# Kernel tuning notes

Measured on AMD Instinct MI355X. Metric: run time of the kernel, lower is better.

The kernel has to match this reference:

```python
import jax, jax.numpy as jnp
import numpy as np

D_MODEL = 768
NUM_HEADS = 12
HEAD_DIM = D_MODEL // NUM_HEADS  # 64, also rotary dim
INTERMEDIATE = 1152
WINDOW = 128          # config.local_attention (layer_id=1 -> local layer)
ROPE_BASE = 10000.0   # local_rope_theta
EPS = 1e-5


def layer_norm_nocenter(x, gamma):
    # keras LayerNormalization(center=False): mean-subtract, no beta
    mu = jnp.mean(x, axis=-1, keepdims=True)
    var = jnp.var(x, axis=-1, keepdims=True)
    return (x - mu) * jax.lax.rsqrt(var + EPS) * gamma


def rotate_half(x):
    x1, x2 = jnp.split(x, 2, axis=-1)
    return jnp.concatenate([-x2, x1], axis=-1)


def setup_inputs() -> dict:
    key = jax.random.key(0)
    ks = jax.random.split(key, 7)
    B, S = 4, 2048
    hidden_states = jax.random.normal(ks[0], (B, S, D_MODEL), dtype=jnp.float32)
    attention_mask = jnp.zeros((B, 1, S, S), dtype=jnp.float32)  # no padding
    s = 0.02
    attn_norm_gamma = jnp.ones((D_MODEL,), dtype=jnp.float32)
    wqkv = jax.random.normal(ks[1], (D_MODEL, 3 * D_MODEL), dtype=jnp.float32) * s
    wo_attn = jax.random.normal(ks[2], (D_MODEL, D_MODEL), dtype=jnp.float32) * s
    mlp_norm_gamma = jnp.ones((D_MODEL,), dtype=jnp.float32)
    wi = jax.random.normal(ks[3], (D_MODEL, 2 * INTERMEDIATE), dtype=jnp.float32) * s
    wo_mlp = jax.random.normal(ks[4], (INTERMEDIATE, D_MODEL), dtype=jnp.float32) * s
    return {
        'hidden_states': hidden_states,
        'attention_mask': attention_mask,
        'attn_norm_gamma': attn_norm_gamma,
        'wqkv': wqkv,
        'wo_attn': wo_attn,
        'mlp_norm_gamma': mlp_norm_gamma,
        'wi': wi,
        'wo_mlp': wo_mlp,
    }


def reference(hidden_states, attention_mask, attn_norm_gamma, wqkv, wo_attn,
              mlp_norm_gamma, wi, wo_mlp):
    B, S, Dm = hidden_states.shape
    H, Dh = NUM_HEADS, HEAD_DIM

    # RoPE cache (NTKScaling with scaling_factor=1 -> plain RoPE)
    idx = jnp.arange(0, Dh, 2, dtype=jnp.float32)
    inv_freq = 1.0 / (ROPE_BASE ** (idx / Dh))          # [Dh/2]
    t = jnp.arange(S, dtype=jnp.float32)
    freqs = t[:, None] * inv_freq[None, :]              # [S, Dh/2]
    emb = jnp.concatenate([freqs, freqs], axis=-1)      # [S, Dh]
    cos = jnp.cos(emb)[None, None]                      # [1,1,S,Dh]
    sin = jnp.sin(emb)[None, None]

    # combined sliding-window + padding mask
    pos = jnp.arange(S)
    dist = jnp.abs(pos[:, None] - pos[None, :])
    neg = jnp.finfo(jnp.float32).min
    local = jnp.where(dist <= WINDOW // 2, 0.0, neg).astype(jnp.float32)
    mask = attention_mask + local[None, None]           # [B,1,S,S]

    # attention (layer_id != 0 -> pre-norm)
    x = layer_norm_nocenter(hidden_states, attn_norm_gamma)
    qkv = (x @ wqkv).reshape(B, S, 3, H, Dh).transpose(2, 0, 3, 1, 4)
    q, k, v = qkv[0], qkv[1], qkv[2]                    # [B,H,S,Dh]
    q = q * cos + rotate_half(q) * sin
    k = k * cos + rotate_half(k) * sin

    scale = 1.0 / jnp.sqrt(jnp.asarray(Dh, q.dtype))
    scores = jnp.einsum('bhqd,bhkd->bhqk', q, k) * scale + mask
    attn = jax.nn.softmax(scores, axis=-1)
    ctx = jnp.einsum('bhqk,bhkd->bhqd', attn, v)
    attn_out = ctx.transpose(0, 2, 1, 3).reshape(B, S, Dm) @ wo_attn

    h = hidden_states + attn_out

    # GLU MLP: Wi -> split -> gelu(x)*gate -> Wo, residual
    n = layer_norm_nocenter(h, mlp_norm_gamma)
    x_in, gate = jnp.split(n @ wi, 2, axis=-1)
    mlp = jax.nn.gelu(x_in, approximate=False) * gate
    return h + mlp @ wo_mlp
```

## Files before the change

### kernel.cpp

```cpp
#include <hip/hip_runtime.h>
#include <cstdint>
#include <cstddef>

typedef __bf16 bf16;
typedef float f32x4 __attribute__((ext_vector_type(4)));
typedef __bf16 bf16x8 __attribute__((ext_vector_type(8)));
typedef __bf16 bf16x4 __attribute__((ext_vector_type(4)));

#define MFMA16(a, b, c) __builtin_amdgcn_mfma_f32_16x16x32_bf16((a), (b), (c), 0, 0, 0)

__device__ __forceinline__ void gload_lds16(const void* g, void* l) {
  __builtin_amdgcn_global_load_lds((__attribute__((address_space(1))) void*)g,
                                   (__attribute__((address_space(3))) void*)l,
                                   16, 0, 0);
}

__global__ __launch_bounds__(256) void wconv_all(const float* __restrict__ wqkv,
                                                 const float* __restrict__ woa,
                                                 const float* __restrict__ wi,
                                                 const float* __restrict__ wom,
                                                 bf16* __restrict__ wqkvT,
                                                 bf16* __restrict__ woaT,
                                                 bf16* __restrict__ wiIT,
                                                 bf16* __restrict__ womT) {
  int id = blockIdx.x;
  const float* W;
  bf16* Wt;
  int K, N, bx, by;
  bool inter = false;
  if (id < 1728) { W = wqkv; Wt = wqkvT; K = 768; N = 2304; bx = id % 72; by = id / 72; }
  else if (id < 2304) { id -= 1728; W = woa; Wt = woaT; K = 768; N = 768; bx = id % 24; by = id / 24; }
  else if (id < 4032) { id -= 2304; W = wi; Wt = wiIT; K = 768; N = 2304; inter = true; bx = id % 72; by = id / 72; }
  else { id -= 4032; W = wom; Wt = womT; K = 1152; N = 768; bx = id % 24; by = id / 24; }

  __shared__ float tile[32][33];
  const int n0 = bx * 32, k0 = by * 32;
  const int t = threadIdx.x;
  const int c = t & 31, r = t >> 5;
#pragma unroll
  for (int i = 0; i < 4; ++i)
    tile[r + i * 8][c] = W[(size_t)(k0 + r + i * 8) * N + n0 + c];
  __syncthreads();
#pragma unroll
  for (int i = 0; i < 4; ++i) {
    int n = n0 + r + i * 8;
    int nw = inter ? ((n < 1152) ? 2 * n : 2 * (n - 1152) + 1) : n;
    Wt[(size_t)nw * K + k0 + c] = (bf16)tile[c][r + i * 8];
  }
}

__global__ __launch_bounds__(256) void ln_kernel(const float* __restrict__ X,
                                                 const float* __restrict__ gamma,
                                                 bf16* __restrict__ out) {
  const int row = blockIdx.x, t = threadIdx.x;
  const float* xr = X + (size_t)row * 768;
  float v0 = xr[t], v1 = xr[t + 256], v2 = xr[t + 512];
  float s = v0 + v1 + v2;
  float s2 = v0 * v0 + v1 * v1 + v2 * v2;
#pragma unroll
  for (int m = 1; m <= 32; m <<= 1) {
    s += __shfl_xor(s, m, 64);
    s2 += __shfl_xor(s2, m, 64);
  }
  __shared__ float red[8];
  const int w = t >> 6, lane = t & 63;
  if (lane == 0) { red[w] = s; red[4 + w] = s2; }
  __syncthreads();
  s = red[0] + red[1] + red[2] + red[3];
  s2 = red[4] + red[5] + red[6] + red[7];
  const float mu = s * (1.f / 768.f);
  const float var = s2 * (1.f / 768.f) - mu * mu;
  const float rs = rsqrtf(var + 1e-5f);
  out[(size_t)row * 768 + t] = (bf16)((v0 - mu) * rs * gamma[t]);
  out[(size_t)row * 768 + t + 256] = (bf16)((v1 - mu) * rs * gamma[t + 256]);
  out[(size_t)row * 768 + t + 512] = (bf16)((v2 - mu) * rs * gamma[t + 512]);
}

template <int BM, bool RES, typename TOUT>
__global__ __launch_bounds__(256) void gemm_bt(const bf16* __restrict__ A,
                                               const bf16* __restrict__ Bt,
                                               const float* __restrict__ Res,
                                               TOUT* __restrict__ C, int M, int N, int K) {
  constexpr int MT = BM / 32;
  __shared__ __align__(16) bf16 As[BM * 64];
  __shared__ __align__(16) bf16 Bs[128 * 64];
  const int t = threadIdx.x;
  const int lane = t & 63;
  const int w = t >> 6;
  const int wm = w >> 1, wn = w & 1;
  const int row0 = blockIdx.y * BM, col0 = blockIdx.x * 128;
  const int rm = lane & 15, qd = lane >> 4;
  f32x4 acc[MT][4] = {};
  for (int k0 = 0; k0 < K; k0 += 64) {
#pragma unroll
    for (int i = 0; i < BM / 32; ++i) {
      int c = i * 256 + t;
      int r = c >> 3, j = (c & 7) ^ (r & 7);
      gload_lds16(A + (size_t)(row0 + r) * K + (k0 + j * 8), &As[c * 8]);
    }
#pragma unroll
    for (int i = 0; i < 4; ++i) {
      int c = i * 256 + t;
      int r = c >> 3, j = (c & 7) ^ (r & 7);
      gload_lds16(Bt + (size_t)(col0 + r) * K + (k0 + j * 8), &Bs[c * 8]);
    }
    __syncthreads();
#pragma unroll
    for (int kb = 0; kb < 2; ++kb) {
      bf16x8 af[MT], bfr[4];
#pragma unroll
      for (int mt = 0; mt < MT; ++mt) {
        int r = wm * (MT * 16) + mt * 16 + rm;
        af[mt] = *(const bf16x8*)&As[r * 64 + (((kb * 4 + qd) ^ (r & 7)) * 8)];
      }
#pragma unroll
      for (int nt = 0; nt < 4; ++nt) {
        int r = wn * 64 + nt * 16 + rm;
        bfr[nt] = *(const bf16x8*)&Bs[r * 64 + (((kb * 4 + qd) ^ (r & 7)) * 8)];
      }
#pragma unroll
      for (int mt = 0; mt < MT; ++mt)
#pragma unroll
        for (int nt = 0; nt < 4; ++nt)
          acc[mt][nt] = MFMA16(af[mt], bfr[nt], acc[mt][nt]);
    }
    __syncthreads();
  }
#pragma unroll
  for (int mt = 0; mt < MT; ++mt)
#pragma unroll
    for (int nt = 0; nt < 4; ++nt) {
      const int gc = col0 + wn * 64 + nt * 16 + rm;
#pragma unroll
      for (int r = 0; r < 4; ++r) {
        const int gr = row0 + wm * (MT * 16) + mt * 16 + qd * 4 + r;
        float v = acc[mt][nt][r];
        const size_t idx = (size_t)gr * N + gc;
        if (RES) v += Res[idx];
        C[idx] = (TOUT)v;
      }
    }
}

__global__ __launch_bounds__(256) void gemm_wi(const bf16* __restrict__ A,
                                               const bf16* __restrict__ Bt,
                                               bf16* __restrict__ outp) {
  __shared__ __align__(16) bf16 As[128 * 64];
  __shared__ __align__(16) bf16 Bs[128 * 64];
  const int t = threadIdx.x;
  const int lane = t & 63;
  const int w = t >> 6;
  const int wm = w >> 1, wn = w & 1;
  const int row0 = blockIdx.y * 128, col0 = blockIdx.x * 128;
  const int rm = lane & 15, qd = lane >> 4;
  f32x4 acc[4][4] = {};
  for (int k0 = 0; k0 < 768; k0 += 64) {
#pragma unroll
    for (int i = 0; i < 4; ++i) {
      int c = i * 256 + t;
      int r = c >> 3, j = (c & 7) ^ (r & 7);
      gload_lds16(A + (size_t)(row0 + r) * 768 + (k0 + j * 8), &As[c * 8]);
      gload_lds16(Bt + (size_t)(col0 + r) * 768 + (k0 + j * 8), &Bs[c * 8]);
    }
    __syncthreads();
#pragma unroll
    for (int kb = 0; kb < 2; ++kb) {
      bf16x8 af[4], bfr[4];
#pragma unroll
      for (int mt = 0; mt < 4; ++mt) {
        int r = wm * 64 + mt * 16 + rm;
        af[mt] = *(const bf16x8*)&As[r * 64 + (((kb * 4 + qd) ^ (r & 7)) * 8)];
      }
#pragma unroll
      for (int nt = 0; nt < 4; ++nt) {
        int r = wn * 64 + nt * 16 + rm;
        bfr[nt] = *(const bf16x8*)&Bs[r * 64 + (((kb * 4 + qd) ^ (r & 7)) * 8)];
      }
#pragma unroll
      for (int mt = 0; mt < 4; ++mt)
#pragma unroll
        for (int nt = 0; nt < 4; ++nt)
          acc[mt][nt] = MFMA16(af[mt], bfr[nt], acc[mt][nt]);
    }
    __syncthreads();
  }
#pragma unroll
  for (int mt = 0; mt < 4; ++mt)
#pragma unroll
    for (int nt = 0; nt < 4; ++nt) {
      const int ci = col0 + wn * 64 + nt * 16 + rm;
#pragma unroll
      for (int r = 0; r < 4; ++r) {
        const int gr = row0 + wm * 64 + mt * 16 + qd * 4 + r;
        float v = acc[mt][nt][r];
        float other = __shfl_xor(v, 1, 64);
        if ((rm & 1) == 0) {
          float x = v, g = other;
          float ge = 0.5f * x * (1.0f + erff(x * 0.70710678118654752f));
          outp[(size_t)gr * 1152 + (ci >> 1)] = (bf16)(ge * g);
        }
      }
    }
}

__global__ __launch_bounds__(256) void gemm_qkv(const bf16* __restrict__ A,
                                                const bf16* __restrict__ Bt,
                                                bf16* __restrict__ Qb,
                                                bf16* __restrict__ Kb,
                                                bf16* __restrict__ Vt) {
  __shared__ __align__(16) bf16 SM[17408];
  bf16* As = SM;
  bf16* Bs = SM + 8192;

  const int t = threadIdx.x;
  const int lane = t & 63;
  const int w = t >> 6;
  const int wm = w >> 1, wn = w & 1;
  const int row0 = blockIdx.y * 128, col0 = blockIdx.x * 128;
  const int rm = lane & 15, qd = lane >> 4;
  f32x4 acc[4][4] = {};
  for (int k0 = 0; k0 < 768; k0 += 64) {
#pragma unroll
    for (int i = 0; i < 4; ++i) {
      int c = i * 256 + t;
      int r = c >> 3, j = (c & 7) ^ (r & 7);
      gload_lds16(A + (size_t)(row0 + r) * 768 + (k0 + j * 8), &As[c * 8]);
      gload_lds16(Bt + (size_t)(col0 + r) * 768 + (k0 + j * 8), &Bs[c * 8]);
    }
    __syncthreads();
#pragma unroll
    for (int kb = 0; kb < 2; ++kb) {
      bf16x8 af[4], bfr[4];
#pragma unroll
      for (int mt = 0; mt < 4; ++mt) {
        int r = wm * 64 + mt * 16 + rm;
        af[mt] = *(const bf16x8*)&As[r * 64 + (((kb * 4 + qd) ^ (r & 7)) * 8)];
      }
#pragma unroll
      for (int nt = 0; nt < 4; ++nt) {
        int r = wn * 64 + nt * 16 + rm;
        bfr[nt] = *(const bf16x8*)&Bs[r * 64 + (((kb * 4 + qd) ^ (r & 7)) * 8)];
      }
#pragma unroll
      for (int mt = 0; mt < 4; ++mt)
#pragma unroll
        for (int nt = 0; nt < 4; ++nt)
          acc[mt][nt] = MFMA16(af[mt], bfr[nt], acc[mt][nt]);
    }
    __syncthreads();
  }

  const int head_id = blockIdx.x * 2 + wn;
  const int typ = blockIdx.x / 6;
  const int b = row0 >> 11;
  const int sblk = row0 & 2047;
  const int sw = sblk + wm * 64;

  if (typ < 2) {
    const int h = head_id - typ * 12;
    const size_t bhbase = (size_t)(b * 12 + h) * 2048;
    bf16* dst = typ ? Kb : Qb;
    float invf[2];
#pragma unroll
    for (int nt = 0; nt < 2; ++nt)
      invf[nt] = exp2f((float)(nt * 16 + rm) * -0.41524101186092029f);
#pragma unroll
    for (int mt = 0; mt < 4; ++mt)
#pragma unroll
      for (int r = 0; r < 4; ++r) {
        int s = sw + mt * 16 + qd * 4 + r;
#pragma unroll
        for (int nt = 0; nt < 2; ++nt) {
          float ang = (float)s * invf[nt];
          float rev = ang * 0.15915494309189535f;
          rev -= floorf(rev);
          float sn = __builtin_amdgcn_sinf(rev);
          float cs = __builtin_amdgcn_cosf(rev);
          float x1 = acc[mt][nt][r], x2 = acc[mt][nt + 2][r];
          int d = nt * 16 + rm;
          dst[(bhbase + s) * 64 + d] = (bf16)(x1 * cs - x2 * sn);
          dst[(bhbase + s) * 64 + d + 32] = (bf16)(x2 * cs + x1 * sn);
        }
      }
  } else {
#pragma unroll
    for (int mt = 0; mt < 4; ++mt)
#pragma unroll
      for (int nt = 0; nt < 4; ++nt) {
        int hd = wn * 64 + nt * 16 + rm;
        int sl = wm * 64 + mt * 16 + qd * 4;
        bf16x4 v4;
#pragma unroll
        for (int r = 0; r < 4; ++r) v4[r] = (bf16)acc[mt][nt][r];
        *(bf16x4*)&SM[hd * 136 + sl] = v4;
      }
    __syncthreads();
    const int h0 = blockIdx.x * 2 - 24;
#pragma unroll
    for (int it = 0; it < 8; ++it) {
      int cc = it * 256 + t;
      int hd = cc >> 4, s8 = (cc & 15) * 8;
      bf16x8 vv = *(const bf16x8*)&SM[hd * 136 + s8];
      size_t grow = (size_t)(b * 12 + h0 + (hd >> 6)) * 64 + (hd & 63);
      *(bf16x8*)&Vt[grow * 2048 + sblk + s8] = vv;
    }
  }
}

__global__ __launch_bounds__(256) void attn_kernel(const bf16* __restrict__ Qb,
                                                   const bf16* __restrict__ Kb,
                                                   const bf16* __restrict__ Vt,
                                                   const float* __restrict__ am,
                                                   bf16* __restrict__ ctx) {
  __shared__ __align__(16) bf16 KP[64 * 200];
  __shared__ __align__(16) bf16 Vts[64 * 192];
  bf16* Ks = KP;
  bf16* Ps = KP;

  const int t = threadIdx.x;
  const int lane = t & 63, w = t >> 6;
  const int rm = lane & 15, qd = lane >> 4;
  const int s0 = blockIdx.x * 64;
  const int bh = blockIdx.y;
  const int b = bh / 12, h = bh - b * 12;
  const size_t baseQ = (size_t)bh * 2048;

#pragma unroll
  for (int i = 0; i < 6; ++i) {
    int c = i * 256 + t;
    int r = c >> 3, j = (c & 7) ^ (r & 7);
    int key = min(max(s0 - 64 + r, 0), 2047);
    gload_lds16(Kb + (baseQ + key) * 64 + j * 8, &Ks[c * 8]);
  }
#pragma unroll
  for (int i = 0; i < 6; ++i) {
    int c = i * 256 + t;
    int r = c / 24, jl = c - r * 24;
    int j = (jl & 24) | ((jl & 7) ^ (r & 7));
    int k0 = min(max(s0 - 64 + j * 8, 0), 2040);
    gload_lds16(Vt + ((size_t)bh * 64 + r) * 2048 + k0, &Vts[c * 8]);
  }

  bf16x8 aq[2];
#pragma unroll
  for (int kb = 0; kb < 2; ++kb)
    aq[kb] = *(const bf16x8*)&Qb[(baseQ + s0 + w * 16 + rm) * 64 + kb * 32 + qd * 8];

  float msk[12][4];
#pragma unroll
  for (int nt = 0; nt < 12; ++nt) {
    int key = s0 - 64 + nt * 16 + rm;
#pragma unroll
    for (int r = 0; r < 4; ++r) {
      int qpos = s0 + w * 16 + qd * 4 + r;
      bool valid = (key >= 0) && (key < 2048) && (key - qpos <= 64) && (qpos - key <= 64);
      msk[nt][r] = valid ? am[((size_t)b * 2048 + qpos) * 2048 + key] : -3e38f;
    }
  }
  __syncthreads();

  f32x4 sc[12];
#pragma unroll
  for (int nt = 0; nt < 12; ++nt) {
    f32x4 a = {0.f, 0.f, 0.f, 0.f};
#pragma unroll
    for (int kb = 0; kb < 2; ++kb) {
      int r = nt * 16 + rm;
      bf16x8 bk = *(const bf16x8*)&Ks[r * 64 + (((kb * 4 + qd) ^ (rm & 7)) * 8)];
      a = MFMA16(aq[kb], bk, a);
    }
    sc[nt] = a;
  }

  float mx[4] = {-3e38f, -3e38f, -3e38f, -3e38f};
#pragma unroll
  for (int nt = 0; nt < 12; ++nt)
#pragma unroll
    for (int r = 0; r < 4; ++r) {
      float v = (msk[nt][r] <= -2.9e38f) ? -3e38f : sc[nt][r] * 0.125f + msk[nt][r];
      sc[nt][r] = v;
      mx[r] = fmaxf(mx[r], v);
    }
#pragma unroll
  for (int r = 0; r < 4; ++r)
#pragma unroll
    for (int m = 1; m <= 8; m <<= 1) mx[r] = fmaxf(mx[r], __shfl_xor(mx[r], m, 64));
  float sum[4] = {0.f, 0.f, 0.f, 0.f};
#pragma unroll
  for (int nt = 0; nt < 12; ++nt)
#pragma unroll
    for (int r = 0; r < 4; ++r) {
      float p = (sc[nt][r] > -1e37f) ? __expf(sc[nt][r] - mx[r]) : 0.f;
      sc[nt][r] = p;
      sum[r] += p;
    }
#pragma unroll
  for (int r = 0; r < 4; ++r)
#pragma unroll
    for (int m = 1; m <= 8; m <<= 1) sum[r] += __shfl_xor(sum[r], m, 64);
  float inv[4];
#pragma unroll
  for (int r = 0; r < 4; ++r) inv[r] = 1.f / sum[r];

  __syncthreads();

#pragma unroll
  for (int nt = 0; nt < 12; ++nt)
#pragma unroll
    for (int r = 0; r < 4; ++r)
      Ps[(w * 16 + qd * 4 + r) * 200 + nt * 16 + rm] = (bf16)(sc[nt][r] * inv[r]);

  f32x4 o[4] = {};
#pragma unroll
  for (int ks = 0; ks < 6; ++ks) {
    bf16x8 ap = *(const bf16x8*)&Ps[(w * 16 + rm) * 200 + ks * 32 + qd * 8];
#pragma unroll
    for (int nt = 0; nt < 4; ++nt) {
      int kc = ks * 4 + qd;
      bf16x8 bv = *(const bf16x8*)&Vts[(nt * 16 + rm) * 192 +
                                       (((kc & 24) | ((kc & 7) ^ (rm & 7))) * 8)];
      o[nt] = MFMA16(ap, bv, o[nt]);
    }
  }
#pragma unroll
  for (int nt = 0; nt < 4; ++nt)
#pragma unroll
    for (int r = 0; r < 4; ++r) {
      int q_ = s0 + w * 16 + qd * 4 + r;
      ctx[((size_t)(b * 2048 + q_)) * 768 + h * 64 + nt * 16 + rm] = (bf16)o[nt][r];
    }
}

extern "C" void kernel_launch(void* const* d_in, const int* in_sizes, int n_in,
                              void* d_out, int out_size, void* d_ws, size_t ws_size,
                              hipStream_t stream) {
  (void)in_sizes; (void)n_in; (void)out_size; (void)ws_size;
  const float* hidden = (const float*)d_in[0];
  const float* amask = (const float*)d_in[1];
  const float* g1 = (const float*)d_in[2];
  const float* wqkv = (const float*)d_in[3];
  const float* woa = (const float*)d_in[4];
  const float* g2 = (const float*)d_in[5];
  const float* wi = (const float*)d_in[6];
  const float* wom = (const float*)d_in[7];
  float* out = (float*)d_out;

  char* p = (char*)d_ws;
  size_t o = 0;
  auto take = [&](size_t bytes) {
    char* r = p + o;
    o = (o + bytes + 255) & ~(size_t)255;
    return r;
  };
  bf16* wqkvT = (bf16*)take((size_t)2304 * 768 * 2);
  bf16* woaT = (bf16*)take((size_t)768 * 768 * 2);
  bf16* wiIT = (bf16*)take((size_t)2304 * 768 * 2);
  bf16* womT = (bf16*)take((size_t)768 * 1152 * 2);
  bf16* xn = (bf16*)take((size_t)8192 * 768 * 2);
  bf16* Qb = (bf16*)take((size_t)98304 * 64 * 2);
  bf16* Kb = (bf16*)take((size_t)98304 * 64 * 2);
  bf16* Vt = (bf16*)take((size_t)98304 * 64 * 2);
  bf16* ctxb = (bf16*)take((size_t)8192 * 768 * 2);
  float* hbuf = (float*)take((size_t)8192 * 768 * 4);
  bf16* mlp = (bf16*)take((size_t)8192 * 1152 * 2);

  wconv_all<<<4896, 256, 0, stream>>>(wqkv, woa, wi, wom, wqkvT, woaT, wiIT, womT);

  ln_kernel<<<8192, 256, 0, stream>>>(hidden, g1, xn);
  gemm_qkv<<<dim3(18, 64), 256, 0, stream>>>(xn, wqkvT, Qb, Kb, Vt);
  attn_kernel<<<dim3(32, 48), 256, 0, stream>>>(Qb, Kb, Vt, amask, ctxb);
  gemm_bt<64, true, float><<<dim3(6, 128), 256, 0, stream>>>(ctxb, woaT, hidden, hbuf,
                                                             8192, 768, 768);

  ln_kernel<<<8192, 256, 0, stream>>>(hbuf, g2, xn);
  gemm_wi<<<dim3(18, 64), 256, 0, stream>>>(xn, wiIT, mlp);
  gemm_bt<64, true, float><<<dim3(6, 128), 256, 0, stream>>>(mlp, womT, hbuf, out,
                                                             8192, 768, 1152);
}
```

Before: 342.7 us.

## Unfuse GEGLU from Wi GEMM and swap grid axes for row-major block order

Removes the fused Wi GEMM+GEGLU kernel and replaces it with a plain bf16 GEMM that writes the full 2304-wide projection, followed by a separate elementwise GEGLU kernel. The interleaved weight permutation goes away. All GEMM grids are transposed so blockIdx.x walks M and blockIdx.y walks N, which changes which blocks run together and how they share cached tiles. The unfused path adds an extra 8192x2304 bf16 intermediate write and read plus one more launch, in exchange for a simpler epilogue that no longer needs shuffles.

```diff
diff --git a/kernel.cpp b/kernel.cpp
--- a/kernel.cpp
+++ b/kernel.cpp
@@ -21,16 +21,15 @@
                                                  const float* __restrict__ wom,
                                                  bf16* __restrict__ wqkvT,
                                                  bf16* __restrict__ woaT,
-                                                 bf16* __restrict__ wiIT,
+                                                 bf16* __restrict__ wiT,
                                                  bf16* __restrict__ womT) {
   int id = blockIdx.x;
   const float* W;
   bf16* Wt;
   int K, N, bx, by;
-  bool inter = false;
   if (id < 1728) { W = wqkv; Wt = wqkvT; K = 768; N = 2304; bx = id % 72; by = id / 72; }
   else if (id < 2304) { id -= 1728; W = woa; Wt = woaT; K = 768; N = 768; bx = id % 24; by = id / 24; }
-  else if (id < 4032) { id -= 2304; W = wi; Wt = wiIT; K = 768; N = 2304; inter = true; bx = id % 72; by = id / 72; }
+  else if (id < 4032) { id -= 2304; W = wi; Wt = wiT; K = 768; N = 2304; bx = id % 72; by = id / 72; }
   else { id -= 4032; W = wom; Wt = womT; K = 1152; N = 768; bx = id % 24; by = id / 24; }
 
   __shared__ float tile[32][33];
@@ -42,11 +41,8 @@
     tile[r + i * 8][c] = W[(size_t)(k0 + r + i * 8) * N + n0 + c];
   __syncthreads();
 #pragma unroll
-  for (int i = 0; i < 4; ++i) {
-    int n = n0 + r + i * 8;
-    int nw = inter ? ((n < 1152) ? 2 * n : 2 * (n - 1152) + 1) : n;
-    Wt[(size_t)nw * K + k0 + c] = (bf16)tile[c][r + i * 8];
-  }
+  for (int i = 0; i < 4; ++i)
+    Wt[(size_t)(n0 + r + i * 8) * K + k0 + c] = (bf16)tile[c][r + i * 8];
 }
 
 __global__ __launch_bounds__(256) void ln_kernel(const float* __restrict__ X,
@@ -88,7 +84,7 @@
   const int lane = t & 63;
   const int w = t >> 6;
   const int wm = w >> 1, wn = w & 1;
-  const int row0 = blockIdx.y * BM, col0 = blockIdx.x * 128;
+  const int row0 = blockIdx.x * BM, col0 = blockIdx.y * 128;
   const int rm = lane & 15, qd = lane >> 4;
   f32x4 acc[MT][4] = {};
   for (int k0 = 0; k0 < K; k0 += 64) {
@@ -138,67 +134,6 @@
         const size_t idx = (size_t)gr * N + gc;
         if (RES) v += Res[idx];
         C[idx] = (TOUT)v;
-      }
-    }
-}
-
-__global__ __launch_bounds__(256) void gemm_wi(const bf16* __restrict__ A,
-                                               const bf16* __restrict__ Bt,
-                                               bf16* __restrict__ outp) {
-  __shared__ __align__(16) bf16 As[128 * 64];
-  __shared__ __align__(16) bf16 Bs[128 * 64];
-  const int t = threadIdx.x;
-  const int lane = t & 63;
-  const int w = t >> 6;
-  const int wm = w >> 1, wn = w & 1;
-  const int row0 = blockIdx.y * 128, col0 = blockIdx.x * 128;
-  const int rm = lane & 15, qd = lane >> 4;
-  f32x4 acc[4][4] = {};
-  for (int k0 = 0; k0 < 768; k0 += 64) {
-#pragma unroll
-    for (int i = 0; i < 4; ++i) {
-      int c = i * 256 + t;
-      int r = c >> 3, j = (c & 7) ^ (r & 7);
-      gload_lds16(A + (size_t)(row0 + r) * 768 + (k0 + j * 8), &As[c * 8]);
-      gload_lds16(Bt + (size_t)(col0 + r) * 768 + (k0 + j * 8), &Bs[c * 8]);
-    }
-    __syncthreads();
-#pragma unroll
-    for (int kb = 0; kb < 2; ++kb) {
-      bf16x8 af[4], bfr[4];
-#pragma unroll
-      for (int mt = 0; mt < 4; ++mt) {
-        int r = wm * 64 + mt * 16 + rm;
-        af[mt] = *(const bf16x8*)&As[r * 64 + (((kb * 4 + qd) ^ (r & 7)) * 8)];
-      }
-#pragma unroll
-      for (int nt = 0; nt < 4; ++nt) {
-        int r = wn * 64 + nt * 16 + rm;
-        bfr[nt] = *(const bf16x8*)&Bs[r * 64 + (((kb * 4 + qd) ^ (r & 7)) * 8)];
-      }
-#pragma unroll
-      for (int mt = 0; mt < 4; ++mt)
-#pragma unroll
-        for (int nt = 0; nt < 4; ++nt)
-          acc[mt][nt] = MFMA16(af[mt], bfr[nt], acc[mt][nt]);
-    }
-    __syncthreads();
-  }
-#pragma unroll
-  for (int mt = 0; mt < 4; ++mt)
-#pragma unroll
-    for (int nt = 0; nt < 4; ++nt) {
-      const int ci = col0 + wn * 64 + nt * 16 + rm;
-#pragma unroll
-      for (int r = 0; r < 4; ++r) {
-        const int gr = row0 + wm * 64 + mt * 16 + qd * 4 + r;
-        float v = acc[mt][nt][r];
-        float other = __shfl_xor(v, 1, 64);
-        if ((rm & 1) == 0) {
-          float x = v, g = other;
-          float ge = 0.5f * x * (1.0f + erff(x * 0.70710678118654752f));
-          outp[(size_t)gr * 1152 + (ci >> 1)] = (bf16)(ge * g);
-        }
       }
     }
 }
@@ -216,7 +151,7 @@
   const int lane = t & 63;
   const int w = t >> 6;
   const int wm = w >> 1, wn = w & 1;
-  const int row0 = blockIdx.y * 128, col0 = blockIdx.x * 128;
+  const int row0 = blockIdx.x * 128, col0 = blockIdx.y * 128;
   const int rm = lane & 15, qd = lane >> 4;
   f32x4 acc[4][4] = {};
   for (int k0 = 0; k0 < 768; k0 += 64) {
@@ -250,8 +185,8 @@
     __syncthreads();
   }
 
-  const int head_id = blockIdx.x * 2 + wn;
-  const int typ = blockIdx.x / 6;
+  const int head_id = blockIdx.y * 2 + wn;
+  const int typ = blockIdx.y / 6;
   const int b = row0 >> 11;
   const int sblk = row0 & 2047;
   const int sw = sblk + wm * 64;
@@ -295,7 +230,7 @@
         *(bf16x4*)&SM[hd * 136 + sl] = v4;
       }
     __syncthreads();
-    const int h0 = blockIdx.x * 2 - 24;
+    const int h0 = blockIdx.y * 2 - 24;
 #pragma unroll
     for (int it = 0; it < 8; ++it) {
       int cc = it * 256 + t;
@@ -429,6 +364,16 @@
       int q_ = s0 + w * 16 + qd * 4 + r;
       ctx[((size_t)(b * 2048 + q_)) * 768 + h * 64 + nt * 16 + rm] = (bf16)o[nt][r];
     }
+}
+
+__global__ __launch_bounds__(128) void geglu_kernel(const bf16* __restrict__ X,
+                                                    bf16* __restrict__ out) {
+  const int row = blockIdx.y;
+  const int c = blockIdx.x * 128 + threadIdx.x;
+  const bf16* xr = X + (size_t)row * 2304;
+  float x = (float)xr[c], g = (float)xr[1152 + c];
+  float ge = 0.5f * x * (1.0f + erff(x * 0.70710678118654752f));
+  out[(size_t)row * 1152 + c] = (bf16)(ge * g);
 }
 
 extern "C" void kernel_launch(void* const* d_in, const int* in_sizes, int n_in,
@@ -454,7 +399,7 @@
   };
   bf16* wqkvT = (bf16*)take((size_t)2304 * 768 * 2);
   bf16* woaT = (bf16*)take((size_t)768 * 768 * 2);
-  bf16* wiIT = (bf16*)take((size_t)2304 * 768 * 2);
+  bf16* wiT = (bf16*)take((size_t)2304 * 768 * 2);
   bf16* womT = (bf16*)take((size_t)768 * 1152 * 2);
   bf16* xn = (bf16*)take((size_t)8192 * 768 * 2);
   bf16* Qb = (bf16*)take((size_t)98304 * 64 * 2);
@@ -462,18 +407,21 @@
   bf16* Vt = (bf16*)take((size_t)98304 * 64 * 2);
   bf16* ctxb = (bf16*)take((size_t)8192 * 768 * 2);
   float* hbuf = (float*)take((size_t)8192 * 768 * 4);
+  bf16* mlpx = (bf16*)take((size_t)8192 * 2304 * 2);
   bf16* mlp = (bf16*)take((size_t)8192 * 1152 * 2);
 
-  wconv_all<<<4896, 256, 0, stream>>>(wqkv, woa, wi, wom, wqkvT, woaT, wiIT, womT);
+  wconv_all<<<4896, 256, 0, stream>>>(wqkv, woa, wi, wom, wqkvT, woaT, wiT, womT);
 
   ln_kernel<<<8192, 256, 0, stream>>>(hidden, g1, xn);
-  gemm_qkv<<<dim3(18, 64), 256, 0, stream>>>(xn, wqkvT, Qb, Kb, Vt);
+  gemm_qkv<<<dim3(64, 18), 256, 0, stream>>>(xn, wqkvT, Qb, Kb, Vt);
   attn_kernel<<<dim3(32, 48), 256, 0, stream>>>(Qb, Kb, Vt, amask, ctxb);
-  gemm_bt<64, true, float><<<dim3(6, 128), 256, 0, stream>>>(ctxb, woaT, hidden, hbuf,
+  gemm_bt<64, true, float><<<dim3(128, 6), 256, 0, stream>>>(ctxb, woaT, hidden, hbuf,
                                                              8192, 768, 768);
 
   ln_kernel<<<8192, 256, 0, stream>>>(hbuf, g2, xn);
-  gemm_wi<<<dim3(18, 64), 256, 0, stream>>>(xn, wiIT, mlp);
-  gemm_bt<64, true, float><<<dim3(6, 128), 256, 0, stream>>>(mlp, womT, hbuf, out,
+  gemm_bt<128, false, bf16><<<dim3(64, 18), 256, 0, stream>>>(xn, wiT, nullptr, mlpx,
+                                                              8192, 2304, 768);
+  geglu_kernel<<<dim3(9, 8192), 128, 0, stream>>>(mlpx, mlp);
+  gemm_bt<64, true, float><<<dim3(128, 6), 256, 0, stream>>>(mlp, womT, hbuf, out,
                                                              8192, 768, 1152);
 }
```

Measured after the change: 330.5 us. 3.5% less time.
